# Kernel optimization log

Hardware: AMD Instinct MI355X
Metric: run time of the kernel (lower is better)

## Reference

```python
import jax, jax.numpy as jnp
import numpy as np

N, D, H, B, K = 65536, 64, 128, 16, 16
EPS = 0.0

def setup_inputs() -> dict:
    key = jax.random.key(0)
    ks = jax.random.split(key, 5)
    x = jax.random.normal(ks[0], (N, D), dtype=jnp.float32)
    pos = jax.random.normal(ks[1], (N, 3), dtype=jnp.float32)
    batch = (jnp.arange(N, dtype=jnp.int32) // (N // B)).astype(jnp.int32)
    W1 = jax.random.normal(ks[2], (D, H), dtype=jnp.float32) * (1.0 / np.sqrt(D))
    b1 = jnp.zeros((H,), dtype=jnp.float32)
    W2 = jax.random.normal(ks[3], (H, D), dtype=jnp.float32) * (1.0 / np.sqrt(H))
    b2 = jnp.zeros((D,), dtype=jnp.float32)
    return {"x": x, "pos": pos, "batch": batch, "W1": W1, "b1": b1, "W2": W2, "b2": b2}

def reference(x, pos, batch, W1, b1, W2, b2):
    # batch is assumed contiguous with B equal segments of n nodes each
    n = N // B
    pos_s = pos.reshape(B, n, 3)
    x_s = x.reshape(B, n, D)
    # pairwise squared distances per segment via gram trick: [B, n, n]
    sq = jnp.sum(pos_s * pos_s, axis=-1)
    d2 = sq[:, :, None] + sq[:, None, :] - 2.0 * jnp.einsum('bic,bjc->bij', pos_s, pos_s)
    # exclude self-loops (loop=False in knn_graph)
    d2 = jnp.where(jnp.eye(n, dtype=bool)[None], jnp.inf, d2)
    # k nearest neighbors per node: indices [B, n, K]
    _, idx = jax.lax.top_k(-d2, K)
    # GIN sum aggregation: gather neighbor features and sum over K
    nb = x_s[jnp.arange(B)[:, None, None], idx]        # [B, n, K, D]
    agg = nb.sum(axis=2).reshape(N, D)                  # [N, D]
    h = (1.0 + EPS) * x + agg
    h = jax.nn.relu(h @ W1 + b1)
    out = h @ W2 + b2
    return out
```

## Files before the change

### kernel.cpp

```cpp
#include <hip/hip_runtime.h>
#include <math.h>

#define DIM  64
#define HID  128
#define NPB  4096
#define KNN  16
#define SEG  1024
#define TSZ  128
#define CAP  12

typedef unsigned long long u64;

__device__ __forceinline__ u64 pack_key(float d, unsigned idx) {
    unsigned u = __float_as_uint(d);
    unsigned m = u ^ ((unsigned)(((int)u) >> 31) | 0x80000000u);
    return ((u64)m << 32) | idx;
}
__device__ __forceinline__ float key_dist(u64 k) {
    unsigned m = (unsigned)(k >> 32);
    unsigned u = (m & 0x80000000u) ? (m ^ 0x80000000u) : ~m;
    return __uint_as_float(u);
}

__device__ __forceinline__ void sorted_insert(u64 (&b)[KNN], u64 key) {
    u64 c = key;
    #pragma unroll
    for (int i = 0; i < KNN; ++i) {
        bool lt = c < b[i];
        u64 lo = lt ? c : b[i];
        u64 hi = lt ? b[i] : c;
        b[i] = lo; c = hi;
    }
}

__device__ __forceinline__ void drain_buf(const u64* bufe, int tid,
                                          u64 (&b)[KNN], int& cnt, float& wv) {
    for (int t = 0; t < CAP; ++t) {
        if (__ballot(t < cnt) == 0ull) break;
        u64 e = bufe[t * 256 + tid];
        unsigned dbits = (unsigned)e;
        unsigned idx   = (unsigned)(e >> 32);
        unsigned m = dbits ^ ((unsigned)(((int)dbits) >> 31) | 0x80000000u);
        u64 key = ((u64)m << 32) | idx;
        if ((t < cnt) && (key < b[KNN - 1])) sorted_insert(b, key);
    }
    cnt = 0;
    wv = key_dist(b[KNN - 1]);
}

struct f2 { float a, b; };
__device__ __forceinline__ f2 f2mul(f2 x, float s) {
    #pragma clang fp contract(off)
    f2 r; r.a = x.a * s; r.b = x.b * s; return r;
}
__device__ __forceinline__ f2 f2add(f2 x, f2 y) {
    #pragma clang fp contract(off)
    f2 r; r.a = x.a + y.a; r.b = x.b + y.b; return r;
}
__device__ __forceinline__ f2 f2adds(f2 x, float s) {
    #pragma clang fp contract(off)
    f2 r; r.a = s + x.a; r.b = s + x.b; return r;
}
__device__ __forceinline__ f2 f2sub(f2 x, f2 y) {
    #pragma clang fp contract(off)
    f2 r; r.a = x.a - y.a; r.b = x.b - y.b; return r;
}

template<bool CHECK>
__device__ __forceinline__ void knn_scan(
    const float* __restrict__ pos, int bbase, int segbase, int qlocal, int l,
    float qx, float qy, float qz, float qs,
    float* tx, float* ty, float* tz, float* ts,
    u64* bufe, int tid, u64 (&b)[KNN])
{
    #pragma clang fp contract(off)
    int cnt = 0;
    float wv;

    {
        #pragma unroll
        for (int m = 0; m < 2; ++m) {
            int t = (m << 6) + l;
            int g = (bbase + segbase + t) * 3;
            float ax = pos[g], ay = pos[g + 1], az = pos[g + 2];
            tx[t] = ax; ty[t] = ay; tz[t] = az;
            ts[t] = (ax * ax + ay * ay) + az * az;
        }
    }

    #pragma unroll
    for (int k = 0; k < KNN; ++k) b[k] = 0xFFFFFFFFFFFFFFFFull;
    for (int jj = 0; jj < KNN; ++jj) {
        float ax = tx[jj], ay = ty[jj], az = tz[jj], as = ts[jj];
        float dot = (ax * qx + ay * qy) + az * qz;
        float d2  = (qs + as) - 2.0f * dot;
        int cj = segbase + jj;
        if (cj == qlocal) d2 = INFINITY;
        sorted_insert(b, pack_key(d2, (unsigned)cj));
    }
    wv = key_dist(b[KNN - 1]);

    int jstart = KNN;
    for (int tb = 0; tb < SEG; tb += TSZ) {
        if (tb > 0) {
            #pragma unroll
            for (int m = 0; m < 2; ++m) {
                int t = (m << 6) + l;
                int g = (bbase + segbase + tb + t) * 3;
                float ax = pos[g], ay = pos[g + 1], az = pos[g + 2];
                tx[t] = ax; ty[t] = ay; tz[t] = az;
                ts[t] = (ax * ax + ay * ay) + az * az;
            }
        }
        for (int j = jstart; j < TSZ; j += 4) {
            float4 X = *(const float4*)(tx + j);
            float4 Y = *(const float4*)(ty + j);
            float4 Z = *(const float4*)(tz + j);
            float4 S = *(const float4*)(ts + j);
            const int c0 = segbase + tb + j;

            {
                f2 Px = {X.x, X.y}, Py = {Y.x, Y.y}, Pz = {Z.x, Z.y}, Ps = {S.x, S.y};
                f2 dot = f2add(f2add(f2mul(Px, qx), f2mul(Py, qy)), f2mul(Pz, qz));
                f2 s1 = f2adds(Ps, qs);
                f2 d2 = f2sub(s1, f2mul(dot, 2.0f));
                if (CHECK) {
                    if (c0     == qlocal) d2.a = INFINITY;
                    if (c0 + 1 == qlocal) d2.b = INFINITY;
                }
                if (d2.a <= wv) {
                    bufe[cnt * 256 + tid] =
                        ((u64)(unsigned)(c0) << 32) | __float_as_uint(d2.a);
                    ++cnt;
                }
                if (d2.b <= wv) {
                    bufe[cnt * 256 + tid] =
                        ((u64)(unsigned)(c0 + 1) << 32) | __float_as_uint(d2.b);
                    ++cnt;
                }
            }
            {
                f2 Px = {X.z, X.w}, Py = {Y.z, Y.w}, Pz = {Z.z, Z.w}, Ps = {S.z, S.w};
                f2 dot = f2add(f2add(f2mul(Px, qx), f2mul(Py, qy)), f2mul(Pz, qz));
                f2 s1 = f2adds(Ps, qs);
                f2 d2 = f2sub(s1, f2mul(dot, 2.0f));
                if (CHECK) {
                    if (c0 + 2 == qlocal) d2.a = INFINITY;
                    if (c0 + 3 == qlocal) d2.b = INFINITY;
                }
                if (d2.a <= wv) {
                    bufe[cnt * 256 + tid] =
                        ((u64)(unsigned)(c0 + 2) << 32) | __float_as_uint(d2.a);
                    ++cnt;
                }
                if (d2.b <= wv) {
                    bufe[cnt * 256 + tid] =
                        ((u64)(unsigned)(c0 + 3) << 32) | __float_as_uint(d2.b);
                    ++cnt;
                }
            }

            if (__ballot(cnt >= CAP - 4) != 0ull)
                drain_buf(bufe, tid, b, cnt, wv);
        }
        jstart = 0;
    }
    drain_buf(bufe, tid, b, cnt, wv);
}

__global__ __launch_bounds__(256, 4) void knn_agg(
    const float* __restrict__ x, const float* __restrict__ pos,
    float* __restrict__ agg_out)
{
    __shared__ u64 smem[4096];

    const int tid = threadIdx.x;
    const int w   = tid >> 6;
    const int l   = tid & 63;

    const int qb     = blockIdx.x;
    const int batch  = qb >> 6;
    const int bbase  = batch << 12;
    const int qlocal = ((qb & 63) << 6) + l;
    const int qglob  = bbase + qlocal;

    float* tilef = (float*)smem;
    float* tx = tilef + w * 512;
    float* ty = tx + TSZ;
    float* tz = tx + 2 * TSZ;
    float* ts = tx + 3 * TSZ;
    u64* bufe = smem + 1024;

    float qx, qy, qz, qs;
    {
        #pragma clang fp contract(off)
        qx = pos[3 * qglob + 0];
        qy = pos[3 * qglob + 1];
        qz = pos[3 * qglob + 2];
        qs = (qx * qx + qy * qy) + qz * qz;
    }

    u64 b[KNN];
    const int segbase = w << 10;
    const int wself   = (qb & 63) >> 4;
    if (w == wself)
        knn_scan<true >(pos, bbase, segbase, qlocal, l, qx, qy, qz, qs,
                        tx, ty, tz, ts, bufe, tid, b);
    else
        knn_scan<false>(pos, bbase, segbase, qlocal, l, qx, qy, qz, qs,
                        tx, ty, tz, ts, bufe, tid, b);

    __syncthreads();

    u64* kb = smem;
    #pragma unroll
    for (int k = 0; k < KNN; ++k) {
        int slot = (w << 4) + k;
        kb[(l << 6) + (slot ^ (l & 31))] = b[k];
    }
    __syncthreads();

    if (tid < 64) {
        u64 m2[KNN];
        #pragma unroll
        for (int c = 0; c < KNN; ++c)
            m2[c] = kb[(tid << 6) + (c ^ (tid & 31))];
        for (int c = KNN; c < 64; ++c) {
            u64 kk = kb[(tid << 6) + (c ^ (tid & 31))];
            if (kk < m2[KNN - 1]) sorted_insert(m2, kk);
        }
        int* mi = (int*)smem;
        #pragma unroll
        for (int k = 0; k < KNN; ++k)
            mi[tid * 17 + k] = (int)(m2[k] & 0xFFFFFFFFull);
    }
    __syncthreads();

    {
        const int* mi = (const int*)smem;
        const int r  = tid >> 2;
        const int p  = tid & 3;
        const int q  = (qb << 6) + r;
        const int cb = p << 4;

        int idxs[KNN];
        #pragma unroll
        for (int k = 0; k < KNN; ++k) idxs[k] = mi[r * 17 + k];

        float4 a0 = *(const float4*)(x + (size_t)q * DIM + cb + 0);
        float4 a1 = *(const float4*)(x + (size_t)q * DIM + cb + 4);
        float4 a2 = *(const float4*)(x + (size_t)q * DIM + cb + 8);
        float4 a3 = *(const float4*)(x + (size_t)q * DIM + cb + 12);

        #pragma unroll 4
        for (int k = 0; k < KNN; ++k) {
            const float* nr = x + (size_t)(bbase + idxs[k]) * DIM + cb;
            float4 v0 = *(const float4*)(nr + 0);
            float4 v1 = *(const float4*)(nr + 4);
            float4 v2 = *(const float4*)(nr + 8);
            float4 v3 = *(const float4*)(nr + 12);
            a0.x += v0.x; a0.y += v0.y; a0.z += v0.z; a0.w += v0.w;
            a1.x += v1.x; a1.y += v1.y; a1.z += v1.z; a1.w += v1.w;
            a2.x += v2.x; a2.y += v2.y; a2.z += v2.z; a2.w += v2.w;
            a3.x += v3.x; a3.y += v3.y; a3.z += v3.z; a3.w += v3.w;
        }

        float* o = agg_out + (size_t)q * DIM + cb;
        *(float4*)(o + 0)  = a0;
        *(float4*)(o + 4)  = a1;
        *(float4*)(o + 8)  = a2;
        *(float4*)(o + 12) = a3;
    }
}

__global__ __launch_bounds__(256, 3) void mlp(
    const float* __restrict__ W1, const float* __restrict__ b1,
    const float* __restrict__ W2, const float* __restrict__ b2,
    float* __restrict__ io)
{
    __shared__ float sm[8192 + 32 * 132];
    float* wl = sm;
    float* hl = sm + 8192;

    const int tid = threadIdx.x;
    const int r   = tid >> 3;
    const int p   = tid & 7;
    const int row = blockIdx.x * 32 + r;

    for (int e = tid; e < HID * DIM; e += 256) wl[e] = W1[e];
    __syncthreads();

    float4 x4[16];
    {
        const float4* xr = (const float4*)(io + (size_t)row * DIM);
        #pragma unroll
        for (int i = 0; i < 16; ++i) x4[i] = xr[i];
    }

    {
        float acc[16];
        #pragma unroll
        for (int c = 0; c < 16; ++c) acc[c] = 0.0f;
        const int jb = p << 4;

        #pragma unroll
        for (int kk = 0; kk < 16; ++kk) {
            float4 xv = x4[kk];
            #pragma unroll
            for (int s = 0; s < 4; ++s) {
                const int k = 4 * kk + s;
                const float xs2 = (s == 0) ? xv.x : (s == 1) ? xv.y : (s == 2) ? xv.z : xv.w;
                const float4* wr = (const float4*)(wl + k * HID + jb);
                float4 w0 = wr[0], w1 = wr[1], w2 = wr[2], w3 = wr[3];
                acc[0]  = fmaf(xs2, w0.x, acc[0]);  acc[1]  = fmaf(xs2, w0.y, acc[1]);
                acc[2]  = fmaf(xs2, w0.z, acc[2]);  acc[3]  = fmaf(xs2, w0.w, acc[3]);
                acc[4]  = fmaf(xs2, w1.x, acc[4]);  acc[5]  = fmaf(xs2, w1.y, acc[5]);
                acc[6]  = fmaf(xs2, w1.z, acc[6]);  acc[7]  = fmaf(xs2, w1.w, acc[7]);
                acc[8]  = fmaf(xs2, w2.x, acc[8]);  acc[9]  = fmaf(xs2, w2.y, acc[9]);
                acc[10] = fmaf(xs2, w2.z, acc[10]); acc[11] = fmaf(xs2, w2.w, acc[11]);
                acc[12] = fmaf(xs2, w3.x, acc[12]); acc[13] = fmaf(xs2, w3.y, acc[13]);
                acc[14] = fmaf(xs2, w3.z, acc[14]); acc[15] = fmaf(xs2, w3.w, acc[15]);
            }
        }
        #pragma unroll
        for (int c = 0; c < 16; ++c) {
            float h = acc[c] + b1[jb + c];
            hl[r * 132 + jb + c] = fmaxf(h, 0.0f);
        }
    }
    __syncthreads();

    for (int e = tid; e < HID * DIM; e += 256) wl[e] = W2[e];
    __syncthreads();

    {
        float acc[8];
        #pragma unroll
        for (int c = 0; c < 8; ++c) acc[c] = 0.0f;
        const int cbb = p << 3;

        #pragma unroll 4
        for (int jj = 0; jj < 32; ++jj) {
            float4 hv = *(const float4*)(hl + r * 132 + 4 * jj);
            #pragma unroll
            for (int s = 0; s < 4; ++s) {
                const int j = 4 * jj + s;
                const float h = (s == 0) ? hv.x : (s == 1) ? hv.y : (s == 2) ? hv.z : hv.w;
                const float4* wr = (const float4*)(wl + j * DIM + cbb);
                float4 w0 = wr[0], w1 = wr[1];
                acc[0] = fmaf(h, w0.x, acc[0]); acc[1] = fmaf(h, w0.y, acc[1]);
                acc[2] = fmaf(h, w0.z, acc[2]); acc[3] = fmaf(h, w0.w, acc[3]);
                acc[4] = fmaf(h, w1.x, acc[4]); acc[5] = fmaf(h, w1.y, acc[5]);
                acc[6] = fmaf(h, w1.z, acc[6]); acc[7] = fmaf(h, w1.w, acc[7]);
            }
        }

        float4 bv0 = *(const float4*)(b2 + cbb);
        float4 bv1 = *(const float4*)(b2 + cbb + 4);
        float4 r0 = make_float4(acc[0] + bv0.x, acc[1] + bv0.y,
                                acc[2] + bv0.z, acc[3] + bv0.w);
        float4 r1 = make_float4(acc[4] + bv1.x, acc[5] + bv1.y,
                                acc[6] + bv1.z, acc[7] + bv1.w);
        float* o = io + (size_t)row * DIM + cbb;
        *(float4*)(o + 0) = r0;
        *(float4*)(o + 4) = r1;
    }
}

extern "C" void kernel_launch(void* const* d_in, const int* in_sizes, int n_in,
                              void* d_out, int out_size, void* d_ws, size_t ws_size,
                              hipStream_t stream) {
    (void)in_sizes; (void)n_in; (void)d_ws; (void)ws_size; (void)out_size;
    const float* x   = (const float*)d_in[0];
    const float* pos = (const float*)d_in[1];
    const float* W1  = (const float*)d_in[3];
    const float* b1  = (const float*)d_in[4];
    const float* W2  = (const float*)d_in[5];
    const float* b2  = (const float*)d_in[6];
    float* out = (float*)d_out;

    knn_agg<<<dim3(1024), dim3(256), 0, stream>>>(x, pos, out);
    mlp<<<dim3(2048), dim3(256), 0, stream>>>(W1, b1, W2, b2, out);
}
```

Baseline: 407.7 us.

## Share kNN pruning threshold across warps and rewrite MLP as per-row fused loop

The kNN scan now keeps separate float distance and int index arrays instead of packed 64-bit keys. It publishes each warp's current 16th-best distance to a shared per-query atomicMin threshold, so all four warps scanning different segments prune candidates with the tightest bound seen so far. The cross-warp merge switches to a transposed float/int layout. The MLP is replaced by a one-row-per-thread kernel that fuses both layers, reading a transposed copy of W1 made by a new prep kernel and weights from global/constant memory. This trades shared-memory weight reuse for large register arrays (64+64 floats) at only 256 blocks, which risks low occupancy and spilling.

```diff
diff --git a/kernel.cpp b/kernel.cpp
--- a/kernel.cpp
+++ b/kernel.cpp
@@ -3,49 +3,40 @@
 
 #define DIM  64
 #define HID  128
-#define NPB  4096
 #define KNN  16
 #define SEG  1024
 #define TSZ  128
 #define CAP  12
 
 typedef unsigned long long u64;
-
-__device__ __forceinline__ u64 pack_key(float d, unsigned idx) {
-    unsigned u = __float_as_uint(d);
-    unsigned m = u ^ ((unsigned)(((int)u) >> 31) | 0x80000000u);
-    return ((u64)m << 32) | idx;
-}
-__device__ __forceinline__ float key_dist(u64 k) {
-    unsigned m = (unsigned)(k >> 32);
-    unsigned u = (m & 0x80000000u) ? (m ^ 0x80000000u) : ~m;
-    return __uint_as_float(u);
-}
-
-__device__ __forceinline__ void sorted_insert(u64 (&b)[KNN], u64 key) {
-    u64 c = key;
+#define INF_BITS 0x7F800000u
+
+__device__ __forceinline__ void ins16(float (&bd)[KNN], int (&bi)[KNN],
+                                      float d, int g) {
+    float cd = d; int ci = g;
     #pragma unroll
     for (int i = 0; i < KNN; ++i) {
-        bool lt = c < b[i];
-        u64 lo = lt ? c : b[i];
-        u64 hi = lt ? b[i] : c;
-        b[i] = lo; c = hi;
+        bool lt = cd < bd[i];
+        float dl = lt ? cd : bd[i];
+        float dh = lt ? bd[i] : cd;
+        int   il = lt ? ci : bi[i];
+        int   ih = lt ? bi[i] : ci;
+        bd[i] = dl; bi[i] = il; cd = dh; ci = ih;
     }
 }
 
 __device__ __forceinline__ void drain_buf(const u64* bufe, int tid,
-                                          u64 (&b)[KNN], int& cnt, float& wv) {
+        float (&bd)[KNN], int (&bi)[KNN], int& cnt,
+        unsigned* thrU, int l) {
     for (int t = 0; t < CAP; ++t) {
         if (__ballot(t < cnt) == 0ull) break;
         u64 e = bufe[t * 256 + tid];
-        unsigned dbits = (unsigned)e;
-        unsigned idx   = (unsigned)(e >> 32);
-        unsigned m = dbits ^ ((unsigned)(((int)dbits) >> 31) | 0x80000000u);
-        u64 key = ((u64)m << 32) | idx;
-        if ((t < cnt) && (key < b[KNN - 1])) sorted_insert(b, key);
+        float d = __uint_as_float((unsigned)e);
+        int   g = (int)(e >> 32);
+        if ((t < cnt) && (d < bd[KNN - 1])) ins16(bd, bi, d, g);
     }
     cnt = 0;
-    wv = key_dist(b[KNN - 1]);
+    atomicMin(&thrU[l], __float_as_uint(bd[KNN - 1]));
 }
 
 struct f2 { float a, b; };
@@ -71,34 +62,34 @@
     const float* __restrict__ pos, int bbase, int segbase, int qlocal, int l,
     float qx, float qy, float qz, float qs,
     float* tx, float* ty, float* tz, float* ts,
-    u64* bufe, int tid, u64 (&b)[KNN])
+    u64* bufe, unsigned* thrU, volatile unsigned* thrv, int tid,
+    float (&bd)[KNN], int (&bi)[KNN])
 {
     #pragma clang fp contract(off)
     int cnt = 0;
-    float wv;
-
-    {
-        #pragma unroll
-        for (int m = 0; m < 2; ++m) {
-            int t = (m << 6) + l;
-            int g = (bbase + segbase + t) * 3;
-            float ax = pos[g], ay = pos[g + 1], az = pos[g + 2];
-            tx[t] = ax; ty[t] = ay; tz[t] = az;
-            ts[t] = (ax * ax + ay * ay) + az * az;
-        }
-    }
-
-    #pragma unroll
-    for (int k = 0; k < KNN; ++k) b[k] = 0xFFFFFFFFFFFFFFFFull;
+
+    #pragma unroll
+    for (int m = 0; m < 2; ++m) {
+        int t = (m << 6) + l;
+        int g = (bbase + segbase + t) * 3;
+        float ax = pos[g], ay = pos[g + 1], az = pos[g + 2];
+        tx[t] = ax; ty[t] = ay; tz[t] = az;
+        ts[t] = (ax * ax + ay * ay) + az * az;
+    }
+
+    __syncthreads();
+
+    #pragma unroll
+    for (int k = 0; k < KNN; ++k) { bd[k] = INFINITY; bi[k] = 0x7FFFFFFF; }
     for (int jj = 0; jj < KNN; ++jj) {
         float ax = tx[jj], ay = ty[jj], az = tz[jj], as = ts[jj];
         float dot = (ax * qx + ay * qy) + az * qz;
         float d2  = (qs + as) - 2.0f * dot;
         int cj = segbase + jj;
         if (cj == qlocal) d2 = INFINITY;
-        sorted_insert(b, pack_key(d2, (unsigned)cj));
-    }
-    wv = key_dist(b[KNN - 1]);
+        ins16(bd, bi, d2, cj);
+    }
+    atomicMin(&thrU[l], __float_as_uint(bd[KNN - 1]));
 
     int jstart = KNN;
     for (int tb = 0; tb < SEG; tb += TSZ) {
@@ -113,66 +104,55 @@
             }
         }
         for (int j = jstart; j < TSZ; j += 4) {
+            float tl = __uint_as_float(thrv[l]);
             float4 X = *(const float4*)(tx + j);
             float4 Y = *(const float4*)(ty + j);
             float4 Z = *(const float4*)(tz + j);
             float4 S = *(const float4*)(ts + j);
             const int c0 = segbase + tb + j;
 
-            {
-                f2 Px = {X.x, X.y}, Py = {Y.x, Y.y}, Pz = {Z.x, Z.y}, Ps = {S.x, S.y};
+            {   f2 Px = {X.x, X.y}, Py = {Y.x, Y.y}, Pz = {Z.x, Z.y}, Ps = {S.x, S.y};
                 f2 dot = f2add(f2add(f2mul(Px, qx), f2mul(Py, qy)), f2mul(Pz, qz));
-                f2 s1 = f2adds(Ps, qs);
-                f2 d2 = f2sub(s1, f2mul(dot, 2.0f));
+                f2 d2  = f2sub(f2adds(Ps, qs), f2mul(dot, 2.0f));
                 if (CHECK) {
                     if (c0     == qlocal) d2.a = INFINITY;
                     if (c0 + 1 == qlocal) d2.b = INFINITY;
                 }
-                if (d2.a <= wv) {
+                if (d2.a <= tl) {
                     bufe[cnt * 256 + tid] =
-                        ((u64)(unsigned)(c0) << 32) | __float_as_uint(d2.a);
-                    ++cnt;
-                }
-                if (d2.b <= wv) {
+                        ((u64)(unsigned)c0 << 32) | __float_as_uint(d2.a); ++cnt; }
+                if (d2.b <= tl) {
                     bufe[cnt * 256 + tid] =
-                        ((u64)(unsigned)(c0 + 1) << 32) | __float_as_uint(d2.b);
-                    ++cnt;
-                }
+                        ((u64)(unsigned)(c0 + 1) << 32) | __float_as_uint(d2.b); ++cnt; }
             }
-            {
-                f2 Px = {X.z, X.w}, Py = {Y.z, Y.w}, Pz = {Z.z, Z.w}, Ps = {S.z, S.w};
+            {   f2 Px = {X.z, X.w}, Py = {Y.z, Y.w}, Pz = {Z.z, Z.w}, Ps = {S.z, S.w};
                 f2 dot = f2add(f2add(f2mul(Px, qx), f2mul(Py, qy)), f2mul(Pz, qz));
-                f2 s1 = f2adds(Ps, qs);
-                f2 d2 = f2sub(s1, f2mul(dot, 2.0f));
+                f2 d2  = f2sub(f2adds(Ps, qs), f2mul(dot, 2.0f));
                 if (CHECK) {
                     if (c0 + 2 == qlocal) d2.a = INFINITY;
                     if (c0 + 3 == qlocal) d2.b = INFINITY;
                 }
-                if (d2.a <= wv) {
+                if (d2.a <= tl) {
                     bufe[cnt * 256 + tid] =
-                        ((u64)(unsigned)(c0 + 2) << 32) | __float_as_uint(d2.a);
-                    ++cnt;
-                }
-                if (d2.b <= wv) {
+                        ((u64)(unsigned)(c0 + 2) << 32) | __float_as_uint(d2.a); ++cnt; }
+                if (d2.b <= tl) {
                     bufe[cnt * 256 + tid] =
-                        ((u64)(unsigned)(c0 + 3) << 32) | __float_as_uint(d2.b);
-                    ++cnt;
-                }
+                        ((u64)(unsigned)(c0 + 3) << 32) | __float_as_uint(d2.b); ++cnt; }
             }
 
             if (__ballot(cnt >= CAP - 4) != 0ull)
-                drain_buf(bufe, tid, b, cnt, wv);
+                drain_buf(bufe, tid, bd, bi, cnt, thrU, l);
         }
         jstart = 0;
     }
-    drain_buf(bufe, tid, b, cnt, wv);
+    drain_buf(bufe, tid, bd, bi, cnt, thrU, l);
 }
 
 __global__ __launch_bounds__(256, 4) void knn_agg(
     const float* __restrict__ x, const float* __restrict__ pos,
     float* __restrict__ agg_out)
 {
-    __shared__ u64 smem[4096];
+    __shared__ u64 smem[4160];
 
     const int tid = threadIdx.x;
     const int w   = tid >> 6;
@@ -189,7 +169,10 @@
     float* ty = tx + TSZ;
     float* tz = tx + 2 * TSZ;
     float* ts = tx + 3 * TSZ;
-    u64* bufe = smem + 1024;
+    unsigned* thrU = (unsigned*)(tilef + 2048);
+    u64* bufe = smem + 1056;
+
+    if (tid < 64) thrU[tid] = INF_BITS;
 
     float qx, qy, qz, qs;
     {
@@ -200,44 +183,48 @@
         qs = (qx * qx + qy * qy) + qz * qz;
     }
 
-    u64 b[KNN];
+    float bd[KNN]; int bi[KNN];
     const int segbase = w << 10;
     const int wself   = (qb & 63) >> 4;
     if (w == wself)
         knn_scan<true >(pos, bbase, segbase, qlocal, l, qx, qy, qz, qs,
-                        tx, ty, tz, ts, bufe, tid, b);
+                        tx, ty, tz, ts, bufe, thrU, thrU, tid, bd, bi);
     else
         knn_scan<false>(pos, bbase, segbase, qlocal, l, qx, qy, qz, qs,
-                        tx, ty, tz, ts, bufe, tid, b);
+                        tx, ty, tz, ts, bufe, thrU, thrU, tid, bd, bi);
 
     __syncthreads();
 
-    u64* kb = smem;
+    float* md  = (float*)smem;
+    int*  midx = (int*)(smem + 2048);
     #pragma unroll
     for (int k = 0; k < KNN; ++k) {
         int slot = (w << 4) + k;
-        kb[(l << 6) + (slot ^ (l & 31))] = b[k];
+        md[slot * 64 + l]   = bd[k];
+        midx[slot * 64 + l] = bi[k];
     }
     __syncthreads();
 
     if (tid < 64) {
-        u64 m2[KNN];
-        #pragma unroll
-        for (int c = 0; c < KNN; ++c)
-            m2[c] = kb[(tid << 6) + (c ^ (tid & 31))];
+        float bd2[KNN]; int bi2[KNN];
+        #pragma unroll
+        for (int k = 0; k < KNN; ++k) {
+            bd2[k] = md[k * 64 + tid];
+            bi2[k] = midx[k * 64 + tid];
+        }
         for (int c = KNN; c < 64; ++c) {
-            u64 kk = kb[(tid << 6) + (c ^ (tid & 31))];
-            if (kk < m2[KNN - 1]) sorted_insert(m2, kk);
-        }
-        int* mi = (int*)smem;
-        #pragma unroll
-        for (int k = 0; k < KNN; ++k)
-            mi[tid * 17 + k] = (int)(m2[k] & 0xFFFFFFFFull);
+            float d = md[c * 64 + tid];
+            int   g = midx[c * 64 + tid];
+            if (d < bd2[KNN - 1]) ins16(bd2, bi2, d, g);
+        }
+        int* mi2 = (int*)smem;
+        #pragma unroll
+        for (int k = 0; k < KNN; ++k) mi2[k * 64 + tid] = bi2[k];
     }
     __syncthreads();
 
     {
-        const int* mi = (const int*)smem;
+        const int* mi2 = (const int*)smem;
         const int r  = tid >> 2;
         const int p  = tid & 3;
         const int q  = (qb << 6) + r;
@@ -245,7 +232,7 @@
 
         int idxs[KNN];
         #pragma unroll
-        for (int k = 0; k < KNN; ++k) idxs[k] = mi[r * 17 + k];
+        for (int k = 0; k < KNN; ++k) idxs[k] = mi2[k * 64 + r];
 
         float4 a0 = *(const float4*)(x + (size_t)q * DIM + cb + 0);
         float4 a1 = *(const float4*)(x + (size_t)q * DIM + cb + 4);
@@ -273,104 +260,61 @@
     }
 }
 
-__global__ __launch_bounds__(256, 3) void mlp(
-    const float* __restrict__ W1, const float* __restrict__ b1,
+__global__ void prep(const float* __restrict__ W1, float* __restrict__ w1t) {
+    int e = blockIdx.x * 256 + threadIdx.x;
+    int k = e >> 7, j = e & 127;
+    w1t[j * 64 + k] = W1[e];
+}
+
+__global__ __launch_bounds__(256, 1) void mlp(
+    const float* __restrict__ w1t, const float* __restrict__ b1,
     const float* __restrict__ W2, const float* __restrict__ b2,
     float* __restrict__ io)
 {
-    __shared__ float sm[8192 + 32 * 132];
-    float* wl = sm;
-    float* hl = sm + 8192;
-
-    const int tid = threadIdx.x;
-    const int r   = tid >> 3;
-    const int p   = tid & 7;
-    const int row = blockIdx.x * 32 + r;
-
-    for (int e = tid; e < HID * DIM; e += 256) wl[e] = W1[e];
-    __syncthreads();
-
-    float4 x4[16];
+    const int row = blockIdx.x * 256 + threadIdx.x;
+
+    float xv[DIM];
     {
         const float4* xr = (const float4*)(io + (size_t)row * DIM);
         #pragma unroll
-        for (int i = 0; i < 16; ++i) x4[i] = xr[i];
-    }
-
-    {
-        float acc[16];
-        #pragma unroll
-        for (int c = 0; c < 16; ++c) acc[c] = 0.0f;
-        const int jb = p << 4;
-
-        #pragma unroll
-        for (int kk = 0; kk < 16; ++kk) {
-            float4 xv = x4[kk];
-            #pragma unroll
-            for (int s = 0; s < 4; ++s) {
-                const int k = 4 * kk + s;
-                const float xs2 = (s == 0) ? xv.x : (s == 1) ? xv.y : (s == 2) ? xv.z : xv.w;
-                const float4* wr = (const float4*)(wl + k * HID + jb);
-                float4 w0 = wr[0], w1 = wr[1], w2 = wr[2], w3 = wr[3];
-                acc[0]  = fmaf(xs2, w0.x, acc[0]);  acc[1]  = fmaf(xs2, w0.y, acc[1]);
-                acc[2]  = fmaf(xs2, w0.z, acc[2]);  acc[3]  = fmaf(xs2, w0.w, acc[3]);
-                acc[4]  = fmaf(xs2, w1.x, acc[4]);  acc[5]  = fmaf(xs2, w1.y, acc[5]);
-                acc[6]  = fmaf(xs2, w1.z, acc[6]);  acc[7]  = fmaf(xs2, w1.w, acc[7]);
-                acc[8]  = fmaf(xs2, w2.x, acc[8]);  acc[9]  = fmaf(xs2, w2.y, acc[9]);
-                acc[10] = fmaf(xs2, w2.z, acc[10]); acc[11] = fmaf(xs2, w2.w, acc[11]);
-                acc[12] = fmaf(xs2, w3.x, acc[12]); acc[13] = fmaf(xs2, w3.y, acc[13]);
-                acc[14] = fmaf(xs2, w3.z, acc[14]); acc[15] = fmaf(xs2, w3.w, acc[15]);
-            }
-        }
-        #pragma unroll
-        for (int c = 0; c < 16; ++c) {
-            float h = acc[c] + b1[jb + c];
-            hl[r * 132 + jb + c] = fmaxf(h, 0.0f);
-        }
-    }
-    __syncthreads();
-
-    for (int e = tid; e < HID * DIM; e += 256) wl[e] = W2[e];
-    __syncthreads();
-
-    {
-        float acc[8];
-        #pragma unroll
-        for (int c = 0; c < 8; ++c) acc[c] = 0.0f;
-        const int cbb = p << 3;
-
-        #pragma unroll 4
-        for (int jj = 0; jj < 32; ++jj) {
-            float4 hv = *(const float4*)(hl + r * 132 + 4 * jj);
-            #pragma unroll
-            for (int s = 0; s < 4; ++s) {
-                const int j = 4 * jj + s;
-                const float h = (s == 0) ? hv.x : (s == 1) ? hv.y : (s == 2) ? hv.z : hv.w;
-                const float4* wr = (const float4*)(wl + j * DIM + cbb);
-                float4 w0 = wr[0], w1 = wr[1];
-                acc[0] = fmaf(h, w0.x, acc[0]); acc[1] = fmaf(h, w0.y, acc[1]);
-                acc[2] = fmaf(h, w0.z, acc[2]); acc[3] = fmaf(h, w0.w, acc[3]);
-                acc[4] = fmaf(h, w1.x, acc[4]); acc[5] = fmaf(h, w1.y, acc[5]);
-                acc[6] = fmaf(h, w1.z, acc[6]); acc[7] = fmaf(h, w1.w, acc[7]);
-            }
-        }
-
-        float4 bv0 = *(const float4*)(b2 + cbb);
-        float4 bv1 = *(const float4*)(b2 + cbb + 4);
-        float4 r0 = make_float4(acc[0] + bv0.x, acc[1] + bv0.y,
-                                acc[2] + bv0.z, acc[3] + bv0.w);
-        float4 r1 = make_float4(acc[4] + bv1.x, acc[5] + bv1.y,
-                                acc[6] + bv1.z, acc[7] + bv1.w);
-        float* o = io + (size_t)row * DIM + cbb;
-        *(float4*)(o + 0) = r0;
-        *(float4*)(o + 4) = r1;
-    }
+        for (int i = 0; i < 16; ++i) {
+            float4 v = xr[i];
+            xv[4*i] = v.x; xv[4*i+1] = v.y; xv[4*i+2] = v.z; xv[4*i+3] = v.w;
+        }
+    }
+
+    float acc[DIM];
+    #pragma unroll
+    for (int c = 0; c < DIM; ++c) acc[c] = b2[c];
+
+    for (int j = 0; j < HID; ++j) {
+        const float* w1 = w1t + j * DIM;
+        float s0 = 0.f, s1 = 0.f, s2 = 0.f, s3 = 0.f;
+        #pragma unroll
+        for (int c = 0; c < DIM; c += 4) {
+            s0 = fmaf(w1[c + 0], xv[c + 0], s0);
+            s1 = fmaf(w1[c + 1], xv[c + 1], s1);
+            s2 = fmaf(w1[c + 2], xv[c + 2], s2);
+            s3 = fmaf(w1[c + 3], xv[c + 3], s3);
+        }
+        float h = fmaxf((s0 + s1) + (s2 + s3) + b1[j], 0.0f);
+
+        const float* w2 = W2 + j * DIM;
+        #pragma unroll
+        for (int c = 0; c < DIM; ++c)
+            acc[c] = fmaf(h, w2[c], acc[c]);
+    }
+
+    float4* o = (float4*)(io + (size_t)row * DIM);
+    #pragma unroll
+    for (int i = 0; i < 16; ++i)
+        o[i] = make_float4(acc[4*i], acc[4*i+1], acc[4*i+2], acc[4*i+3]);
 }
 
 extern "C" void kernel_launch(void* const* d_in, const int* in_sizes, int n_in,
                               void* d_out, int out_size, void* d_ws, size_t ws_size,
                               hipStream_t stream) {
-    (void)in_sizes; (void)n_in; (void)d_ws; (void)ws_size; (void)out_size;
+    (void)in_sizes; (void)n_in; (void)ws_size; (void)out_size;
     const float* x   = (const float*)d_in[0];
     const float* pos = (const float*)d_in[1];
     const float* W1  = (const float*)d_in[3];
@@ -378,7 +322,9 @@
     const float* W2  = (const float*)d_in[5];
     const float* b2  = (const float*)d_in[6];
     float* out = (float*)d_out;
-
+    float* w1t = (float*)d_ws;
+
+    prep<<<dim3(32), dim3(256), 0, stream>>>(W1, w1t);
     knn_agg<<<dim3(1024), dim3(256), 0, stream>>>(x, pos, out);
-    mlp<<<dim3(2048), dim3(256), 0, stream>>>(W1, b1, W2, b2, out);
-}
+    mlp<<<dim3(256), dim3(256), 0, stream>>>(w1t, b1, W2, b2, out);
+}
```

Measured after the change: 417.3 us. 2.3% more time.
